# Performance work log

Measured on AMD Instinct MI355X. Metric: run time of the kernel, lower is better.

The kernel has to match this reference:

```python
import jax, jax.numpy as jnp
import numpy as np

# Model dims derived from layers=[1024,2048,2048,2048,2048]
B = 4096
SUM_EVEN = 4096  # 0 + 2048 + 2048
SUM_ODD = 4096   # 2048 + 2048
D1 = 2048        # layers[1]: width of Ux
BLK = 2048


def rho(x):
    return jax.nn.sigmoid(4.0 * (x - 0.5))


def make_mask():
    # Staircase block pattern from layer_slices():
    # (rows 0:2048, cols 0:2048), (rows 0:2048, cols 2048:4096), (rows 2048:4096, cols 2048:4096)
    m = np.zeros((SUM_EVEN, SUM_ODD), dtype=np.float32)
    m[0:BLK, 0:BLK] = 1.0
    m[0:BLK, BLK:2 * BLK] = 1.0
    m[BLK:2 * BLK, BLK:2 * BLK] = 1.0
    return jnp.asarray(m)


def setup_inputs() -> dict:
    key = jax.random.key(0)
    k1, k2, k3 = jax.random.split(key, 3)
    xavier_std = 0.02  # ~ sqrt(2/(2048+2048)) per block
    W_mask = make_mask()
    W_tensor = jax.random.normal(k1, (SUM_EVEN, SUM_ODD), jnp.float32) * xavier_std
    W_tensor = W_tensor * W_mask  # enforce staircase sparsity at init
    return {
        "Ux": jax.random.normal(k2, (B, D1), jnp.float32),
        "s": jax.random.normal(k3, (B, SUM_EVEN), jnp.float32),
        "W_tensor": W_tensor,
        "b_even": jnp.zeros((1, SUM_EVEN), jnp.float32),
        "b_odd": jnp.zeros((1, SUM_ODD), jnp.float32),
        "W_mask": W_mask,
    }


def reference(Ux, s, W_tensor, b_even, b_odd, W_mask):
    # s_new = rho(rho(s) @ W + b_odd [+ Ux on first D1 cols]) @ W.T + b_even
    W = W_tensor * W_mask  # masked staircase matrix
    s_odd = rho(s) @ W + b_odd                 # [B, SUM_ODD]
    s_odd = s_odd.at[:, :D1].add(Ux)           # x only feeds first hidden layer
    return rho(s_odd) @ W.T + b_even           # [B, SUM_EVEN]
```

## Files before the change

### kernel.cpp

```cpp
#include <hip/hip_runtime.h>
#include <hip/hip_bf16.h>


#define N_DIM 4096
#define D1_DIM 2048

typedef short short8 __attribute__((ext_vector_type(8)));
typedef float f32x4 __attribute__((ext_vector_type(4)));

__device__ __forceinline__ float rho_f(float x) {
    return 1.0f / (1.0f + __expf(2.0f - 4.0f * x));
}

__device__ __forceinline__ unsigned short f2bf(float x) {
    unsigned int u = __builtin_bit_cast(unsigned int, x);
    u += 0x7fffu + ((u >> 16) & 1u);
    return (unsigned short)(u >> 16);
}

__device__ __forceinline__ void gl_lds16(const unsigned short* g, void* l) {
    __builtin_amdgcn_global_load_lds(
        (const __attribute__((address_space(1))) void*)g,
        (__attribute__((address_space(3))) void*)l, 16, 0, 0);
}

__global__ __launch_bounds__(256) void prep_kernel(
    const float* __restrict__ s, const float* __restrict__ W,
    unsigned short* __restrict__ Rs, unsigned short* __restrict__ Wb,
    unsigned short* __restrict__ WTb) {
    __shared__ unsigned short t[32][33];
    const int id = blockIdx.x;
    if (id < 16384) {
        const int bx = id & 127, by = id >> 7;
        if (by * 32 >= D1_DIM && bx * 32 < D1_DIM) return;
        const int tx = threadIdx.x & 31, ty = threadIdx.x >> 5;
        const int x = bx * 32 + tx;
        #pragma unroll
        for (int r = 0; r < 4; r++) {
            const int y = by * 32 + ty + r * 8;
            const size_t idx = (size_t)y * N_DIM + x;
            const unsigned short b = f2bf(W[idx]);
            Wb[idx] = b;
            t[ty + r * 8][tx] = b;
        }
        __syncthreads();
        #pragma unroll
        for (int r = 0; r < 4; r++) {
            const int yy = ty + r * 8;
            WTb[(size_t)(bx * 32 + yy) * N_DIM + (by * 32 + tx)] = t[tx][yy];
        }
    } else {
        const int n8 = (N_DIM * N_DIM) / 8;
        const int stride = 2048 * 256;
        for (int i = (id - 16384) * 256 + threadIdx.x; i < n8; i += stride) {
            float4 a = ((const float4*)s)[2 * i];
            float4 b = ((const float4*)s)[2 * i + 1];
            unsigned int r0 = f2bf(rho_f(a.x)) | ((unsigned int)f2bf(rho_f(a.y)) << 16);
            unsigned int r1 = f2bf(rho_f(a.z)) | ((unsigned int)f2bf(rho_f(a.w)) << 16);
            unsigned int r2 = f2bf(rho_f(b.x)) | ((unsigned int)f2bf(rho_f(b.y)) << 16);
            unsigned int r3 = f2bf(rho_f(b.z)) | ((unsigned int)f2bf(rho_f(b.w)) << 16);
            uint4 o; o.x = r0; o.y = r1; o.z = r2; o.w = r3;
            ((uint4*)Rs)[i] = o;
        }
    }
}

template<int MODE>
__global__ __launch_bounds__(512, 2) void gemm_kernel(
    const unsigned short* __restrict__ A,
    const unsigned short* __restrict__ Bt,
    void* __restrict__ Out,
    const float* __restrict__ Ux,
    const float* __restrict__ bias) {
    __shared__ __align__(16) char lds[163840];

    const int id = blockIdx.x;
    const int wg = ((id & 7) << 5) | (id >> 3);
    const int by = wg >> 4, bx = wg & 15;
    const int brow = by << 8, bcol = bx << 8;

    const int tid = threadIdx.x;
    const int w = tid >> 6;
    const int L = tid & 63;
    const int wr = w >> 2;
    const int wc = w & 3;
    const int fr = L & 15;
    const int fq = L >> 4;
    const int swz = fr & 7;

    int kbeg, kend;
    if (MODE == 1) { kbeg = 0; kend = (bcol < D1_DIM) ? D1_DIM : N_DIM; }
    else           { kbeg = (bcol < D1_DIM) ? 0 : D1_DIM; kend = N_DIM; }

    const int srl = w * 8 + (L >> 3);
    const int schunk8 = ((L & 7) ^ (L >> 3)) << 3;
    const int wbase = w * 1024;
#define STAGE2(mat, gb, h, kcol, base) do {                                    \
        const unsigned short* g0_ = (mat) +                                    \
            (size_t)((gb) + (h) * 128 + srl) * N_DIM + (kcol) + schunk8;       \
        gl_lds16(g0_, lds + (base) + (h) * 16384 + wbase);                     \
        gl_lds16(g0_ + 64 * N_DIM, lds + (base) + (h) * 16384 + 8192 + wbase); \
    } while (0)

    short8 af0[2][4], af1[2][4], bf0[2][2], bf1[2][2];
#define LDA_Q(ab, qm, dst) do {                                                \
        _Pragma("unroll") for (int s_ = 0; s_ < 2; ++s_)                       \
        _Pragma("unroll") for (int m_ = 0; m_ < 4; ++m_) {                     \
            const int R_ = wr * 128 + (qm) * 64 + m_ * 16 + fr;                \
            dst[s_][m_] = *(const short8*)(lds + (ab) + R_ * 128 +             \
                (((4 * s_ + fq) ^ swz) << 4)); }                               \
    } while (0)
#define LDB_Q(bb, qn, dst) do {                                                \
        _Pragma("unroll") for (int s_ = 0; s_ < 2; ++s_)                       \
        _Pragma("unroll") for (int n_ = 0; n_ < 2; ++n_) {                     \
            const int R_ = wc * 64 + (qn) * 32 + n_ * 16 + fr;                 \
            dst[s_][n_] = *(const short8*)(lds + (bb) + R_ * 128 +             \
                (((4 * s_ + fq) ^ swz) << 4)); }                               \
    } while (0)

    f32x4 acc[8][4];
    #pragma unroll
    for (int i = 0; i < 8; i++)
        #pragma unroll
        for (int j = 0; j < 4; j++)
            acc[i][j] = (f32x4){0.f, 0.f, 0.f, 0.f};

#define MFMA_Q(afr, bfr, qm, qn) do {                                          \
        __builtin_amdgcn_s_setprio(1);                                         \
        _Pragma("unroll") for (int s_ = 0; s_ < 2; ++s_)                       \
        _Pragma("unroll") for (int m_ = 0; m_ < 4; ++m_)                       \
        _Pragma("unroll") for (int n_ = 0; n_ < 2; ++n_)                       \
            acc[(qm) * 4 + m_][(qn) * 2 + n_] =                                \
                __builtin_amdgcn_mfma_f32_16x16x32_bf16(                       \
                    afr[s_][m_], bfr[s_][n_], acc[(qm) * 4 + m_][(qn) * 2 + n_],\
                    0, 0, 0);                                                  \
        __builtin_amdgcn_s_setprio(0);                                         \
    } while (0)

#define SBAR0() __builtin_amdgcn_sched_barrier(0)
#define LGKM(n) do { asm volatile("s_waitcnt lgkmcnt(" #n ")" ::: "memory");   \
                     SBAR0(); } while (0)
#define BAR() __builtin_amdgcn_s_barrier()

    const int nk = (kend - kbeg) >> 6;
    const int km = nk - 1;

    {
        const int k0 = kbeg;
        const int k1 = kbeg + ((1 & km) << 6);
        STAGE2(A, brow, 0, k0, 0);       STAGE2(A, brow, 1, k0, 0);
        STAGE2(Bt, bcol, 0, k0, 98304);  STAGE2(Bt, bcol, 1, k0, 98304);
        STAGE2(A, brow, 0, k1, 32768);   STAGE2(A, brow, 1, k1, 32768);
        STAGE2(Bt, bcol, 0, k1, 131072); STAGE2(Bt, bcol, 1, k1, 131072);
        asm volatile("s_waitcnt vmcnt(8)" ::: "memory");
        BAR();
    }

    int ai = 0, si = 2;
    for (int t = 0; t < nk; ++t) {
        const int aB = ai * 32768;
        const int sA = si * 32768;
        const int bB = 98304 + (t & 1) * 32768;
        const int ka = kbeg + (((t + 2) & km) << 6);

        STAGE2(A, brow, 0, ka, sA);
        STAGE2(A, brow, 1, ka, sA);
        LDA_Q(aB, 0, af0); SBAR0();
        LDB_Q(bB, 0, bf0); SBAR0();
        LDB_Q(bB, 1, bf1); SBAR0();
        LDA_Q(aB, 1, af1); SBAR0();

        LGKM(12);
        MFMA_Q(af0, bf0, 0, 0);
        LGKM(8);
        MFMA_Q(af0, bf1, 0, 1);
        BAR();
        STAGE2(Bt, bcol, 0, ka, bB);
        STAGE2(Bt, bcol, 1, ka, bB);
        LGKM(0);
        MFMA_Q(af1, bf0, 1, 0);
        MFMA_Q(af1, bf1, 1, 1);
        asm volatile("s_waitcnt vmcnt(8)" ::: "memory");
        BAR();
        ai++; if (ai == 3) ai = 0;
        si++; if (si == 3) si = 0;
    }
    asm volatile("s_waitcnt vmcnt(0)" ::: "memory");

    const bool hasUx = (MODE == 1) && (bcol < D1_DIM);
    #pragma unroll
    for (int qm = 0; qm < 2; qm++)
        #pragma unroll
        for (int m = 0; m < 4; m++) {
            const int row0 = brow + wr * 128 + qm * 64 + m * 16 + fq * 4;
            #pragma unroll
            for (int qn = 0; qn < 2; qn++)
                #pragma unroll
                for (int n = 0; n < 2; n++) {
                    const int col = bcol + wc * 64 + qn * 32 + n * 16 + fr;
                    const float bv = bias[col];
                    #pragma unroll
                    for (int r = 0; r < 4; r++) {
                        const int row = row0 + r;
                        float v = acc[qm * 4 + m][qn * 2 + n][r] + bv;
                        if (MODE == 1) {
                            if (hasUx) v += Ux[(size_t)row * D1_DIM + col];
                            ((unsigned short*)Out)[(size_t)row * N_DIM + col] =
                                f2bf(rho_f(v));
                        } else {
                            ((float*)Out)[(size_t)row * N_DIM + col] = v;
                        }
                    }
                }
        }
#undef STAGE2
#undef LDA_Q
#undef LDB_Q
#undef MFMA_Q
#undef SBAR0
#undef LGKM
#undef BAR
}

extern "C" void kernel_launch(void* const* d_in, const int* in_sizes, int n_in,
                              void* d_out, int out_size, void* d_ws, size_t ws_size,
                              hipStream_t stream) {
    const float* Ux     = (const float*)d_in[0];
    const float* s      = (const float*)d_in[1];
    const float* W      = (const float*)d_in[2];
    const float* b_even = (const float*)d_in[3];
    const float* b_odd  = (const float*)d_in[4];

    char* ws = (char*)d_ws;
    const size_t SZ = (size_t)N_DIM * N_DIM * 2;
    unsigned short* Rs  = (unsigned short*)(ws);
    unsigned short* R2  = (unsigned short*)(ws + SZ);
    unsigned short* Wb  = (unsigned short*)(ws + 2 * SZ);
    unsigned short* WTb = (unsigned short*)(ws + 3 * SZ);

    prep_kernel<<<18432, 256, 0, stream>>>(s, W, Rs, Wb, WTb);
    gemm_kernel<1><<<256, 512, 0, stream>>>(Rs, WTb, (void*)R2, Ux, b_odd);
    gemm_kernel<2><<<256, 512, 0, stream>>>(R2, Wb, d_out, Ux, b_even);
}
```

Measured before the change: 264.9 us.

## Double waves per GEMM block to shrink per-wave tile to 64x64

The GEMM workgroup grows from 512 to 1024 threads (16 waves), and each wave now computes a 64x64 sub-tile instead of 128x64. Staging, fragment loads and the MFMA schedule are rewritten around the smaller per-wave tile, with the K-slices processed sequentially. The aim is more waves to hide latency and fewer accumulator registers per wave. In exchange each wave does less data reuse per LDS read, and the launch bounds of 4 blocks of 1024 threads cannot be met with about 160KB of LDS per block.

After: 248.5 us. 6.2% less time.

```diff
diff --git a/kernel.cpp b/kernel.cpp
--- a/kernel.cpp
+++ b/kernel.cpp
@@ -66,7 +66,7 @@
 }
 
 template<int MODE>
-__global__ __launch_bounds__(512, 2) void gemm_kernel(
+__global__ __launch_bounds__(1024, 4) void gemm_kernel(
     const unsigned short* __restrict__ A,
     const unsigned short* __restrict__ Bt,
     void* __restrict__ Out,
@@ -95,45 +95,40 @@
     const int srl = w * 8 + (L >> 3);
     const int schunk8 = ((L & 7) ^ (L >> 3)) << 3;
     const int wbase = w * 1024;
-#define STAGE2(mat, gb, h, kcol, base) do {                                    \
+#define STAGEF(mat, gb, kcol, base) do {                                       \
         const unsigned short* g0_ = (mat) +                                    \
-            (size_t)((gb) + (h) * 128 + srl) * N_DIM + (kcol) + schunk8;       \
-        gl_lds16(g0_, lds + (base) + (h) * 16384 + wbase);                     \
-        gl_lds16(g0_ + 64 * N_DIM, lds + (base) + (h) * 16384 + 8192 + wbase); \
-    } while (0)
-
-    short8 af0[2][4], af1[2][4], bf0[2][2], bf1[2][2];
-#define LDA_Q(ab, qm, dst) do {                                                \
-        _Pragma("unroll") for (int s_ = 0; s_ < 2; ++s_)                       \
+            (size_t)((gb) + srl) * N_DIM + (kcol) + schunk8;                   \
+        gl_lds16(g0_, lds + (base) + wbase);                                   \
+        gl_lds16(g0_ + 128 * N_DIM, lds + (base) + 16384 + wbase);             \
+    } while (0)
+
+    short8 af[2][4], bf[4];
+#define LDA_K(ab, ks) do {                                                     \
         _Pragma("unroll") for (int m_ = 0; m_ < 4; ++m_) {                     \
-            const int R_ = wr * 128 + (qm) * 64 + m_ * 16 + fr;                \
-            dst[s_][m_] = *(const short8*)(lds + (ab) + R_ * 128 +             \
-                (((4 * s_ + fq) ^ swz) << 4)); }                               \
-    } while (0)
-#define LDB_Q(bb, qn, dst) do {                                                \
-        _Pragma("unroll") for (int s_ = 0; s_ < 2; ++s_)                       \
-        _Pragma("unroll") for (int n_ = 0; n_ < 2; ++n_) {                     \
-            const int R_ = wc * 64 + (qn) * 32 + n_ * 16 + fr;                 \
-            dst[s_][n_] = *(const short8*)(lds + (bb) + R_ * 128 +             \
-                (((4 * s_ + fq) ^ swz) << 4)); }                               \
-    } while (0)
-
-    f32x4 acc[8][4];
+            const int R_ = wr * 64 + m_ * 16 + fr;                             \
+            af[ks][m_] = *(const short8*)(lds + (ab) + R_ * 128 +              \
+                ((((ks) * 4 + fq) ^ swz) << 4)); }                             \
+    } while (0)
+#define LDB_K(bb, ks) do {                                                     \
+        _Pragma("unroll") for (int n_ = 0; n_ < 4; ++n_) {                     \
+            const int R_ = wc * 64 + n_ * 16 + fr;                             \
+            bf[n_] = *(const short8*)(lds + (bb) + R_ * 128 +                  \
+                ((((ks) * 4 + fq) ^ swz) << 4)); }                             \
+    } while (0)
+
+    f32x4 acc[4][4];
     #pragma unroll
-    for (int i = 0; i < 8; i++)
+    for (int i = 0; i < 4; i++)
         #pragma unroll
         for (int j = 0; j < 4; j++)
             acc[i][j] = (f32x4){0.f, 0.f, 0.f, 0.f};
 
-#define MFMA_Q(afr, bfr, qm, qn) do {                                          \
+#define MFMA_K(ks) do {                                                        \
         __builtin_amdgcn_s_setprio(1);                                         \
-        _Pragma("unroll") for (int s_ = 0; s_ < 2; ++s_)                       \
         _Pragma("unroll") for (int m_ = 0; m_ < 4; ++m_)                       \
-        _Pragma("unroll") for (int n_ = 0; n_ < 2; ++n_)                       \
-            acc[(qm) * 4 + m_][(qn) * 2 + n_] =                                \
-                __builtin_amdgcn_mfma_f32_16x16x32_bf16(                       \
-                    afr[s_][m_], bfr[s_][n_], acc[(qm) * 4 + m_][(qn) * 2 + n_],\
-                    0, 0, 0);                                                  \
+        _Pragma("unroll") for (int n_ = 0; n_ < 4; ++n_)                       \
+            acc[m_][n_] = __builtin_amdgcn_mfma_f32_16x16x32_bf16(             \
+                af[ks][m_], bf[n_], acc[m_][n_], 0, 0, 0);                     \
         __builtin_amdgcn_s_setprio(0);                                         \
     } while (0)
 
@@ -148,11 +143,9 @@
     {
         const int k0 = kbeg;
         const int k1 = kbeg + ((1 & km) << 6);
-        STAGE2(A, brow, 0, k0, 0);       STAGE2(A, brow, 1, k0, 0);
-        STAGE2(Bt, bcol, 0, k0, 98304);  STAGE2(Bt, bcol, 1, k0, 98304);
-        STAGE2(A, brow, 0, k1, 32768);   STAGE2(A, brow, 1, k1, 32768);
-        STAGE2(Bt, bcol, 0, k1, 131072); STAGE2(Bt, bcol, 1, k1, 131072);
-        asm volatile("s_waitcnt vmcnt(8)" ::: "memory");
+        STAGEF(A, brow, k0, 0);       STAGEF(Bt, bcol, k0, 98304);
+        STAGEF(A, brow, k1, 32768);   STAGEF(Bt, bcol, k1, 131072);
+        asm volatile("s_waitcnt vmcnt(4)" ::: "memory");
         BAR();
     }
 
@@ -163,24 +156,18 @@
         const int bB = 98304 + (t & 1) * 32768;
         const int ka = kbeg + (((t + 2) & km) << 6);
 
-        STAGE2(A, brow, 0, ka, sA);
-        STAGE2(A, brow, 1, ka, sA);
-        LDA_Q(aB, 0, af0); SBAR0();
-        LDB_Q(bB, 0, bf0); SBAR0();
-        LDB_Q(bB, 1, bf1); SBAR0();
-        LDA_Q(aB, 1, af1); SBAR0();
-
-        LGKM(12);
-        MFMA_Q(af0, bf0, 0, 0);
-        LGKM(8);
-        MFMA_Q(af0, bf1, 0, 1);
+        STAGEF(A, brow, ka, sA);
+        LDA_K(aB, 0); SBAR0();
+        LDB_K(bB, 0); SBAR0();
+        LDA_K(aB, 1); SBAR0();
+        LGKM(4);
+        MFMA_K(0);
+        LDB_K(bB, 1); SBAR0();
+        LGKM(0);
+        MFMA_K(1);
         BAR();
-        STAGE2(Bt, bcol, 0, ka, bB);
-        STAGE2(Bt, bcol, 1, ka, bB);
-        LGKM(0);
-        MFMA_Q(af1, bf0, 1, 0);
-        MFMA_Q(af1, bf1, 1, 1);
-        asm volatile("s_waitcnt vmcnt(8)" ::: "memory");
+        STAGEF(Bt, bcol, ka, bB);
+        asm volatile("s_waitcnt vmcnt(4)" ::: "memory");
         BAR();
         ai++; if (ai == 3) ai = 0;
         si++; if (si == 3) si = 0;
@@ -189,34 +176,30 @@
 
     const bool hasUx = (MODE == 1) && (bcol < D1_DIM);
     #pragma unroll
-    for (int qm = 0; qm < 2; qm++)
-        #pragma unroll
-        for (int m = 0; m < 4; m++) {
-            const int row0 = brow + wr * 128 + qm * 64 + m * 16 + fq * 4;
+    for (int m = 0; m < 4; m++) {
+        const int row0 = brow + wr * 64 + m * 16 + fq * 4;
+        #pragma unroll
+        for (int n = 0; n < 4; n++) {
+            const int col = bcol + wc * 64 + n * 16 + fr;
+            const float bv = bias[col];
             #pragma unroll
-            for (int qn = 0; qn < 2; qn++)
-                #pragma unroll
-                for (int n = 0; n < 2; n++) {
-                    const int col = bcol + wc * 64 + qn * 32 + n * 16 + fr;
-                    const float bv = bias[col];
-                    #pragma unroll
-                    for (int r = 0; r < 4; r++) {
-                        const int row = row0 + r;
-                        float v = acc[qm * 4 + m][qn * 2 + n][r] + bv;
-                        if (MODE == 1) {
-                            if (hasUx) v += Ux[(size_t)row * D1_DIM + col];
-                            ((unsigned short*)Out)[(size_t)row * N_DIM + col] =
-                                f2bf(rho_f(v));
-                        } else {
-                            ((float*)Out)[(size_t)row * N_DIM + col] = v;
-                        }
-                    }
+            for (int r = 0; r < 4; r++) {
+                const int row = row0 + r;
+                float v = acc[m][n][r] + bv;
+                if (MODE == 1) {
+                    if (hasUx) v += Ux[(size_t)row * D1_DIM + col];
+                    ((unsigned short*)Out)[(size_t)row * N_DIM + col] =
+                        f2bf(rho_f(v));
+                } else {
+                    ((float*)Out)[(size_t)row * N_DIM + col] = v;
                 }
-        }
-#undef STAGE2
-#undef LDA_Q
-#undef LDB_Q
-#undef MFMA_Q
+            }
+        }
+    }
+#undef STAGEF
+#undef LDA_K
+#undef LDB_K
+#undef MFMA_K
 #undef SBAR0
 #undef LGKM
 #undef BAR
@@ -239,6 +222,6 @@
     unsigned short* WTb = (unsigned short*)(ws + 3 * SZ);
 
     prep_kernel<<<18432, 256, 0, stream>>>(s, W, Rs, Wb, WTb);
-    gemm_kernel<1><<<256, 512, 0, stream>>>(Rs, WTb, (void*)R2, Ux, b_odd);
-    gemm_kernel<2><<<256, 512, 0, stream>>>(R2, Wb, d_out, Ux, b_even);
-}
+    gemm_kernel<1><<<256, 1024, 0, stream>>>(Rs, WTb, (void*)R2, Ux, b_odd);
+    gemm_kernel<2><<<256, 1024, 0, stream>>>(R2, Wb, d_out, Ux, b_even);
+}
```
